# Performance work log

Hardware: AMD Instinct MI355X
Metric: run time of the kernel (lower is better)

## Reference

```python
import jax, jax.numpy as jnp
import numpy as np

N_QUBITS = 14
N_LAYERS = 4
N_CLASSES = 10
BATCH = 1024


def apply_1q(state, gate, wire):
    """Apply a 2x2 gate ([2,2] shared or [B,2,2] batched) to `wire` of state [B,2,...,2]."""
    s = jnp.moveaxis(state, wire + 1, -1)
    shp = s.shape
    s = s.reshape(shp[0], -1, 2)
    if gate.ndim == 3:
        s = jnp.einsum('bij,bkj->bki', gate, s)
    else:
        s = jnp.einsum('ij,bkj->bki', gate, s)
    return jnp.moveaxis(s.reshape(shp), -1, wire + 1)


def apply_cnot(state, c, t):
    s = jnp.moveaxis(state, (c + 1, t + 1), (-2, -1))
    s = jnp.stack([s[..., 0, :], s[..., 1, ::-1]], axis=-2)
    return jnp.moveaxis(s, (-2, -1), (c + 1, t + 1))


def simulate(x, q_params):
    """Batched statevector sim of: RY(x_i) embed -> BasicEntanglerLayers(RX + CNOT ring) -> <Z_i>."""
    B, n = x.shape
    state = jnp.zeros((B,) + (2,) * n, jnp.complex64)
    state = state.at[(slice(None),) + (0,) * n].set(1.0)

    # RY(x_i) on each wire (angles batched per sample)
    c, s = jnp.cos(0.5 * x), jnp.sin(0.5 * x)
    for w in range(n):
        g = jnp.stack([jnp.stack([c[:, w], -s[:, w]], -1),
                       jnp.stack([s[:, w], c[:, w]], -1)], -2).astype(jnp.complex64)  # [B,2,2]
        state = apply_1q(state, g, w)

    # BasicEntanglerLayers: per layer RX(weights[l,i]) on every wire, then CNOT ring
    cw, sw = jnp.cos(0.5 * q_params), jnp.sin(0.5 * q_params)
    n_layers = q_params.shape[0]
    for l in range(n_layers):
        for w in range(n):
            cc = cw[l, w].astype(jnp.complex64)
            isw = (-1j) * sw[l, w].astype(jnp.complex64)
            g = jnp.stack([jnp.stack([cc, isw]), jnp.stack([isw, cc])])  # [2,2] RX
            state = apply_1q(state, g, w)
        if n == 2:
            state = apply_cnot(state, 0, 1)
        else:
            for w in range(n):
                state = apply_cnot(state, w, (w + 1) % n)

    # <Z_i> = P(bit_i=0) - P(bit_i=1)
    p = jnp.abs(state) ** 2  # [B,2,...,2] real
    axes_all = tuple(range(1, n + 1))
    z = []
    for w in range(n):
        pw = jnp.sum(p, axis=tuple(a for a in axes_all if a != w + 1))  # [B,2]
        z.append(pw[:, 0] - pw[:, 1])
    return jnp.stack(z, -1).astype(jnp.float32)  # [B, n]


def setup_inputs() -> dict:
    key = jax.random.key(0)
    k1, k2, k3, k4 = jax.random.split(key, 4)
    x = jax.random.normal(k1, (BATCH, N_QUBITS), dtype=jnp.float32)
    q_params = 0.01 * jax.random.normal(k2, (N_LAYERS, N_QUBITS), dtype=jnp.float32)
    fc_w = jax.random.normal(k3, (N_CLASSES, N_QUBITS), dtype=jnp.float32) / np.sqrt(N_QUBITS)
    fc_b = jax.random.normal(k4, (N_CLASSES,), dtype=jnp.float32) * 0.01
    return {"x": x, "q_params": q_params, "fc_w": fc_w, "fc_b": fc_b}


def reference(x, q_params, fc_w, fc_b):
    q_out = simulate(x, q_params)            # [B, n_qubits]
    logits = q_out @ fc_w.T + fc_b           # [B, n_classes]
    return logits
```

## Files before the change

### kernel.cpp

```cpp
#include <hip/hip_runtime.h>
#include <hip/hip_fp16.h>
#include <math.h>


#define NQ 14
#define NLAYERS 4
#define NCLASSES 10
#define BLOCK 512

typedef _Float16 f16;
typedef _Float16 f16x2 __attribute__((ext_vector_type(2)));
typedef _Float16 f16x4 __attribute__((ext_vector_type(4)));
typedef _Float16 f16x8 __attribute__((ext_vector_type(8)));
typedef float f32x4 __attribute__((ext_vector_type(4)));
typedef unsigned int u32;
typedef u32 u32x2 __attribute__((ext_vector_type(2)));

__device__ __forceinline__ f32x4 mf(f16x8 a, f16x8 b, f32x4 c) {
  return __builtin_amdgcn_mfma_f32_16x16x32_f16(a, b, c, 0, 0, 0);
}
__device__ __forceinline__ f32x4 mf16(f16x4 a, f16x4 b, f32x4 c) {
  return __builtin_amdgcn_mfma_f32_16x16x16f16(a, b, c, 0, 0, 0);
}
__device__ __forceinline__ int swz(int t) { return ((t ^ (t >> 3)) & 7) << 3; }

__device__ __forceinline__ f16x4 cvt4(f32x4 v) {
  u32x2 r;
  r[0] = __builtin_bit_cast(u32, __builtin_amdgcn_cvt_pkrtz(v[0], v[1]));
  r[1] = __builtin_bit_cast(u32, __builtin_amdgcn_cvt_pkrtz(v[2], v[3]));
  return __builtin_bit_cast(f16x4, r);
}
__device__ __forceinline__ u32 dwof(f16x4 v, int k) {
  return __builtin_bit_cast(u32x2, v)[k];
}

__device__ __forceinline__ int finv5(int n) {
  n ^= ((n >> 3) & 1) << 4;
  n ^= ((n >> 2) & 1) << 3;
  n ^= ((n >> 1) & 1) << 2;
  n ^= (n & 1) << 1;
  return n;
}
__device__ __forceinline__ int finv3(int n) {
  n ^= ((n >> 2) & 1) << 3;
  n ^= ((n >> 1) & 1) << 2;
  n ^= (n & 1) << 1;
  return n;
}

__device__ __forceinline__ void build32(f16* Bc, const float* qc, const float* qs,
                                        int base, int tid) {
  const float c0 = qc[base], c1 = qc[base+1], c2 = qc[base+2], c3 = qc[base+3], c4 = qc[base+4];
  const float s0 = qs[base], s1 = qs[base+1], s2 = qs[base+2], s3 = qs[base+3], s4 = qs[base+4];
#pragma unroll
  for (int e = tid; e < 1024; e += BLOCK) {
    const int n = e >> 5, k = e & 31;
    const int d = finv5(n) ^ k;
    float mag = ((d & 1) ? s0 : c0) * ((d & 2) ? s1 : c1);
    mag *= ((d & 4) ? s2 : c2) * ((d & 8) ? s3 : c3);
    mag *= ((d & 16) ? s4 : c4);
    const int t = __popc(d) & 3;
    const f16 v = (f16)((t == 1 || t == 2) ? -mag : mag);
    const int p = 256 * (k >> 3) + 8 * n + (k & 7);
    const bool isreal = !(t & 1);
    Bc[p]        = isreal ? v : (f16)0.f;
    Bc[p + 1024] = isreal ? (f16)0.f : v;
  }
}

__device__ __forceinline__ void buildC2(f16* Cc, const float* qc, const float* qs,
                                        int base, int tid) {
  if (tid < 256) {
    const float c0 = qc[base], c1 = qc[base+1], c2 = qc[base+2], c3 = qc[base+3];
    const float s0 = qs[base], s1 = qs[base+1], s2 = qs[base+2], s3 = qs[base+3];
    const int rp = tid >> 4, k = tid & 15;
    const int d = finv3(rp) ^ k;
    float mag = ((d & 1) ? s0 : c0) * ((d & 2) ? s1 : c1);
    mag *= ((d & 4) ? s2 : c2) * ((d & 8) ? s3 : c3);
    const int t = __popc(d) & 3;
    const f16 v = (f16)((t == 1 || t == 2) ? -mag : mag);
    const bool isreal = !(t & 1);
    const int p = 16 * rp + k;
    Cc[p]       = isreal ? v : (f16)0.f;
    Cc[p + 256] = isreal ? (f16)0.f : v;
    Cc[p + 512] = isreal ? (f16)0.f : (f16)(-v);
  }
}

__device__ __forceinline__ void passA(f16* __restrict__ reP, f16* __restrict__ imP,
                                      const f16* __restrict__ BcR,
                                      f16* __restrict__ BcW, int baseB,
                                      f16* __restrict__ CcW, int baseC,
                                      const float* __restrict__ qc,
                                      const float* __restrict__ qs, int tid) {
  const int lane = tid & 63, wave = tid >> 6;
  const int q = lane >> 4, cc = lane & 15;
  const int n0 = cc, n1 = cc | 16;
  const f16x8 br0 = *(const f16x8*)(BcR + 256 * q + 8 * n0);
  const f16x8 bi0 = *(const f16x8*)(BcR + 1024 + 256 * q + 8 * n0);
  const f16x8 br1 = *(const f16x8*)(BcR + 256 * q + 8 * n1);
  const f16x8 bi1 = *(const f16x8*)(BcR + 1024 + 256 * q + 8 * n1);
  f16x8 Ar[4], Ai[4];
#pragma unroll
  for (int i = 0; i < 4; ++i) {
    const int mt = wave * 4 + i;
    const int pA = mt * 512 + ((128 * q + 8 * cc) ^ swz(mt));
    Ar[i] = *(const f16x8*)(reP + pA);
    Ai[i] = *(const f16x8*)(imP + pA);
  }
  __syncthreads();
  f16x4 outR[8], outI[8];
#pragma unroll
  for (int i = 0; i < 4; ++i) {
    const f16x8 nAi = -Ai[i];
    {
      f32x4 aR = {0.f,0.f,0.f,0.f}, aI = {0.f,0.f,0.f,0.f};
      aR = mf(Ar[i], br0, aR); aR = mf(nAi, bi0, aR);
      aI = mf(Ar[i], bi0, aI); aI = mf(Ai[i], br0, aI);
      outR[i * 2 + 0] = cvt4(aR);
      outI[i * 2 + 0] = cvt4(aI);
    }
    {
      f32x4 aR = {0.f,0.f,0.f,0.f}, aI = {0.f,0.f,0.f,0.f};
      aR = mf(Ar[i], br1, aR); aR = mf(nAi, bi1, aR);
      aI = mf(Ar[i], bi1, aI); aI = mf(Ai[i], br1, aI);
      outR[i * 2 + 1] = cvt4(aR);
      outI[i * 2 + 1] = cvt4(aI);
    }
  }
#pragma unroll
  for (int i = 0; i < 4; ++i) {
    const int mt = wave * 4 + i;
#pragma unroll
    for (int nt = 0; nt < 2; ++nt) {
      const int n5 = nt * 16 + cc;
      const int pS = n5 * 512 +
          ((128 * (2 * (mt & 1) + (q >> 1)) + 8 * (mt >> 1) + 4 * (q & 1)) ^ swz(n5));
      *(f16x4*)(reP + pS) = outR[i * 2 + nt];
      *(f16x4*)(imP + pS) = outI[i * 2 + nt];
    }
  }
  build32(BcW, qc, qs, baseB, tid);
  buildC2(CcW, qc, qs, baseC, tid);
}

template<bool FINAL>
__device__ __forceinline__ void superBC(f16* __restrict__ reP, f16* __restrict__ imP,
                                        const f16* __restrict__ BcR,
                                        const f16* __restrict__ Cc,
                                        f16* __restrict__ BcW, int baseB,
                                        const float* __restrict__ qc,
                                        const float* __restrict__ qs,
                                        int tid, float* __restrict__ zloc) {
  const int lane = tid & 63, wave = tid >> 6;
  const int q = lane >> 4, cc = lane & 15;
  int n0 = cc, n1 = cc | 16;
  if (wave >= 4) { n0 ^= 31; n1 ^= 31; }
  const f16x8 br0 = *(const f16x8*)(BcR + 256 * q + 8 * n0);
  const f16x8 bi0 = *(const f16x8*)(BcR + 1024 + 256 * q + 8 * n0);
  const f16x8 br1 = *(const f16x8*)(BcR + 256 * q + 8 * n1);
  const f16x8 bi1 = *(const f16x8*)(BcR + 1024 + 256 * q + 8 * n1);
  const int r0 = 16 * cc + 4 * q, r1 = 16 * (cc ^ 15) + 4 * q;
  const f16x4 ucr0 = *(const f16x4*)(Cc + r0);
  const f16x4 uci0 = *(const f16x4*)(Cc + 256 + r0);
  const f16x4 ucn0 = *(const f16x4*)(Cc + 512 + r0);
  const f16x4 ucr1 = *(const f16x4*)(Cc + r1);
  const f16x4 uci1 = *(const f16x4*)(Cc + 256 + r1);
  const f16x4 ucn1 = *(const f16x4*)(Cc + 512 + r1);
  f16x8 Ar[4], Ai[4];
#pragma unroll
  for (int i = 0; i < 4; ++i) {
    const int mt = wave * 4 + i;
    const int pA = mt * 512 + ((128 * q + 8 * cc) ^ swz(mt));
    Ar[i] = *(const f16x8*)(reP + pA);
    Ai[i] = *(const f16x8*)(imP + pA);
  }
  if constexpr (!FINAL) __syncthreads();

  f16x4 accR[4][2], accI[4][2];
  float z0b = 0.f, z1b = 0.f, z9b = 0.f, zA = 0.f, zB = 0.f, pt = 0.f;
#pragma unroll
  for (int i = 0; i < 4; ++i) {
    const f16x8 nAi = -Ai[i];
#pragma unroll
    for (int h = 0; h < 2; ++h) {
      const f16x8 br = h ? br1 : br0;
      const f16x8 bi = h ? bi1 : bi0;
      f32x4 aR = {0.f,0.f,0.f,0.f}, aI = {0.f,0.f,0.f,0.f};
      aR = mf(Ar[i], br, aR); aR = mf(nAi, bi, aR);
      aI = mf(Ar[i], bi, aI); aI = mf(Ai[i], br, aI);
      const f16x4 s1r = cvt4(aR), s1i = cvt4(aI);
      const f16x4 ur = h ? ucr1 : ucr0;
      const f16x4 ui = h ? uci1 : uci0;
      const f16x4 un = h ? ucn1 : ucn0;
      f32x4 cR = {0.f,0.f,0.f,0.f}, cI = {0.f,0.f,0.f,0.f};
      cR = mf16(ur, s1r, cR); cR = mf16(un, s1i, cR);
      cI = mf16(ui, s1r, cI); cI = mf16(ur, s1i, cI);
      if constexpr (FINAL) {
        const float p0 = cR[0]*cR[0] + cI[0]*cI[0];
        const float p1 = cR[1]*cR[1] + cI[1]*cI[1];
        const float p2 = cR[2]*cR[2] + cI[2]*cI[2];
        const float p3 = cR[3]*cR[3] + cI[3]*cI[3];
        const float ps = (p0 + p1) + (p2 + p3);
        zA += (p0 - p1) + (p2 - p3);
        zB += (p0 + p1) - (p2 + p3);
        z0b += (i & 1) ? -ps : ps;
        z1b += (i & 2) ? -ps : ps;
        z9b += h ? -ps : ps;
        pt  += ps;
      } else {
        accR[i][h] = cvt4(cR);
        accI[i][h] = cvt4(cI);
      }
    }
  }
  if constexpr (FINAL) {
    zloc[0]  += (q & 2) ? -z0b : z0b;
    zloc[1]  += z1b;
    zloc[2]  += (wave & 1) ? -pt : pt;
    zloc[3]  += (wave & 2) ? -pt : pt;
    zloc[4]  += (wave & 4) ? -pt : pt;
    zloc[5]  += (cc & 1) ? -pt : pt;
    zloc[6]  += (cc & 2) ? -pt : pt;
    zloc[7]  += (cc & 4) ? -pt : pt;
    zloc[8]  += (cc & 8) ? -pt : pt;
    zloc[9]  += z9b;
    zloc[10] += zA;
    zloc[11] += zB;
    zloc[12] += (q & 1) ? -pt : pt;
    zloc[13] += (q & 2) ? -pt : pt;
  } else {
    const u32 selLo = (q & 2) ? 0x01000504u : 0x05040100u;
    const u32 selHi = (q & 2) ? 0x03020706u : 0x07060302u;
    const int ibase = 128 * (wave >> 1) + 4 * (wave & 1);
#pragma unroll
    for (int h = 0; h < 2; ++h) {
#pragma unroll
      for (int j = 0; j < 4; ++j) {
        const int pS = (8 * q + 2 * j + h) * 512 + ibase +
                       8 * (cc ^ (2 * j + h) ^ q);
        const int dj = j >> 1;
        const u32 sel = (j & 1) ? selHi : selLo;
        u32x2 vr, vi;
        vr[0] = __builtin_amdgcn_perm(dwof(accR[1][h], dj), dwof(accR[0][h], dj), sel);
        vr[1] = __builtin_amdgcn_perm(dwof(accR[3][h], dj), dwof(accR[2][h], dj), sel);
        vi[0] = __builtin_amdgcn_perm(dwof(accI[1][h], dj), dwof(accI[0][h], dj), sel);
        vi[1] = __builtin_amdgcn_perm(dwof(accI[3][h], dj), dwof(accI[2][h], dj), sel);
        *(u32x2*)(reP + pS) = vr;
        *(u32x2*)(imP + pS) = vi;
      }
    }
    build32(BcW, qc, qs, baseB, tid);
  }
}

__global__ __launch_bounds__(BLOCK, 4) void qsim_kernel(
    const float* __restrict__ x, const float* __restrict__ qp,
    const float* __restrict__ fcw, const float* __restrict__ fcb,
    float* __restrict__ out) {
  extern __shared__ unsigned char smem[];
  f16* reP = (f16*)smem;
  f16* imP = reP + 16384;
  f16* Bc0 = imP + 16384;
  f16* Bc1 = Bc0 + 2048;
  f16* Cc  = Bc1 + 2048;
  float* qc = (float*)(Cc + 768);
  float* qs = qc + 56;
  float* xc = qs + 56;
  float* xs = xc + 14;

  const int b = blockIdx.x;
  const int tid = threadIdx.x;

  if (tid < NQ) {
    float sv, cv; sincosf(0.5f * x[b * NQ + tid], &sv, &cv);
    xc[tid] = cv; xs[tid] = sv;
  } else if (tid >= 64 && tid < 64 + NLAYERS * NQ) {
    const int k = tid - 64;
    float sv, cv; sincosf(0.5f * qp[k], &sv, &cv);
    qc[k] = cv; qs[k] = sv;
  }
  __syncthreads();

  float* Flo  = (float*)Bc0;
  float* psi  = Flo + 32;
  float* PsiR = psi + 32;
  float* PsiI = PsiR + 32;
  if (tid < 32) {
    float f = 1.f;
#pragma unroll
    for (int j = 0; j < 5; ++j) f *= ((tid >> j) & 1) ? xs[5 + j] : xc[5 + j];
    Flo[tid] = f;
  } else if (tid < 64) {
    const int k = tid - 32;
    float f = 1.f;
#pragma unroll
    for (int j = 0; j < 5; ++j) f *= ((k >> j) & 1) ? xs[j] : xc[j];
    psi[k] = f;
  }
  __syncthreads();
  if (tid < 32) {
    const float c0 = qc[0], c1 = qc[1], c2 = qc[2], c3 = qc[3], c4 = qc[4];
    const float s0 = qs[0], s1 = qs[1], s2 = qs[2], s3 = qs[3], s4 = qs[4];
    const int a = finv5(tid);
    float ar = 0.f, ai = 0.f;
    for (int k = 0; k < 32; ++k) {
      const int d = a ^ k;
      float mag = ((d & 1) ? s0 : c0) * ((d & 2) ? s1 : c1);
      mag *= ((d & 4) ? s2 : c2) * ((d & 8) ? s3 : c3);
      mag *= ((d & 16) ? s4 : c4);
      mag *= psi[k];
      const int t = __popc(d) & 3;
      if (t == 0) ar += mag; else if (t == 1) ai -= mag;
      else if (t == 2) ar -= mag; else ai += mag;
    }
    PsiR[tid] = ar; PsiI[tid] = ai;
  }
  __syncthreads();
  {
    float fhi = 1.f;
#pragma unroll
    for (int j = 0; j < 4; ++j) fhi *= ((tid >> j) & 1) ? xs[10 + j] : xc[10 + j];
    const float cr = fhi * PsiR[tid >> 4], ci = fhi * PsiI[tid >> 4];
    const int t = tid >> 4;
    const int sz = swz(t);
    float Fl[32];
#pragma unroll
    for (int j = 0; j < 32; ++j) Fl[j] = Flo[j];
    __syncthreads();
#pragma unroll
    for (int kb = 0; kb < 4; ++kb) {
      f16x8 hr, hi;
#pragma unroll
      for (int j = 0; j < 8; ++j) {
        const float F = Fl[8 * kb + j];
        hr[j] = (f16)(F * cr);
        hi[j] = (f16)(F * ci);
      }
      const int pb = t * 512 + ((128 * kb + 8 * (tid & 15)) ^ sz);
      *(f16x8*)(reP + pb) = hr;
      *(f16x8*)(imP + pb) = hi;
    }
  }
  build32(Bc0, qc, qs, 0 * NQ + 5, tid);
  buildC2(Cc, qc, qs, 0 * NQ + 10, tid);
  __syncthreads();

  superBC<false>(reP, imP, Bc0, Cc, Bc1, 1 * NQ + 0, qc, qs, tid, nullptr);
  __syncthreads();
#pragma unroll
  for (int l = 1; l < NLAYERS; ++l) {
    passA(reP, imP, Bc1, Bc0, l * NQ + 5, Cc, l * NQ + 10, qc, qs, tid);
    __syncthreads();
    if (l < NLAYERS - 1) {
      superBC<false>(reP, imP, Bc0, Cc, Bc1, (l + 1) * NQ + 0, qc, qs, tid, nullptr);
      __syncthreads();
    }
  }

  float zloc[NQ];
#pragma unroll
  for (int w = 0; w < NQ; ++w) zloc[w] = 0.f;
  superBC<true>(reP, imP, Bc0, Cc, nullptr, 0, qc, qs, tid, zloc);
  __syncthreads();

  float* zpart = (float*)Bc0;
  float* zbuf  = zpart + 112;
#pragma unroll
  for (int w = 0; w < NQ; ++w) {
#pragma unroll
    for (int off = 32; off > 0; off >>= 1)
      zloc[w] += __shfl_down(zloc[w], off, 64);
  }
  const int wave = tid >> 6, lane = tid & 63;
  if (lane == 0) {
#pragma unroll
    for (int w = 0; w < NQ; ++w) zpart[wave * NQ + w] = zloc[w];
  }
  __syncthreads();
  if (tid < NQ) {
    float a = 0.f;
#pragma unroll
    for (int v = 0; v < 8; ++v) a += zpart[v * NQ + tid];
    zbuf[tid] = a;
  }
  __syncthreads();
  if (tid < NCLASSES) {
    float acc = fcb[tid];
#pragma unroll
    for (int w = 0; w < NQ; ++w) acc = fmaf(zbuf[w], fcw[tid * NQ + w], acc);
    out[b * NCLASSES + tid] = acc;
  }
}

extern "C" void kernel_launch(void* const* d_in, const int* in_sizes, int n_in,
                              void* d_out, int out_size, void* d_ws, size_t ws_size,
                              hipStream_t stream) {
  const float* x   = (const float*)d_in[0];
  const float* qp  = (const float*)d_in[1];
  const float* fcw = (const float*)d_in[2];
  const float* fcb = (const float*)d_in[3];
  float* out = (float*)d_out;
  const int B = in_sizes[0] / NQ;

  const size_t shmem = (size_t)(2 * 16384 + 2 * 2048 + 768) * sizeof(f16)
                     + (size_t)(56 + 56 + 14 + 14) * sizeof(float);
  (void)hipFuncSetAttribute((const void*)qsim_kernel,
                            hipFuncAttributeMaxDynamicSharedMemorySize, (int)shmem);
  qsim_kernel<<<B, BLOCK, shmem, stream>>>(x, qp, fcw, fcb, out);
}
```

Measured before the change: 120.5 us.

## Precompute gate matrices in a prologue kernel and load them from global

Moves construction of the batch-independent RX gate matrices (B and C blocks) out of every block into a single-block prologue kernel that writes them to workspace. The main kernel then loads each layer's operands straight from global memory into registers, prefetching the next layer's operands during the current pass. This removes redundant per-block trig and matrix building plus the shared-memory staging, and cuts the LDS footprint, which may allow more blocks per CU. In exchange it adds a second kernel launch and global loads on the critical path.

```diff
diff --git a/kernel.cpp b/kernel.cpp
--- a/kernel.cpp
+++ b/kernel.cpp
@@ -48,58 +48,89 @@
   return n;
 }
 
-__device__ __forceinline__ void build32(f16* Bc, const float* qc, const float* qs,
-                                        int base, int tid) {
-  const float c0 = qc[base], c1 = qc[base+1], c2 = qc[base+2], c3 = qc[base+3], c4 = qc[base+4];
-  const float s0 = qs[base], s1 = qs[base+1], s2 = qs[base+2], s3 = qs[base+3], s4 = qs[base+4];
+__global__ void qsim_build(const float* __restrict__ qp,
+                           f16* __restrict__ gB, f16* __restrict__ gC) {
+  __shared__ float qc[NLAYERS * NQ], qs[NLAYERS * NQ];
+  const int tid = threadIdx.x;
+  if (tid < NLAYERS * NQ) {
+    float sv, cv; sincosf(0.5f * qp[tid], &sv, &cv);
+    qc[tid] = cv; qs[tid] = sv;
+  }
+  __syncthreads();
+#pragma unroll
+  for (int p = 0; p < 7; ++p) {
+    const int l = (p + 1) >> 1;
+    const int base = 14 * l + ((p & 1) ? 0 : 5);
+    const float c0 = qc[base], c1 = qc[base+1], c2 = qc[base+2], c3 = qc[base+3], c4 = qc[base+4];
+    const float s0 = qs[base], s1 = qs[base+1], s2 = qs[base+2], s3 = qs[base+3], s4 = qs[base+4];
+#pragma unroll
+    for (int e = tid; e < 1024; e += BLOCK) {
+      const int n = e >> 5, k = e & 31;
+      const int d = finv5(n) ^ k;
+      float mag = ((d & 1) ? s0 : c0) * ((d & 2) ? s1 : c1);
+      mag *= ((d & 4) ? s2 : c2) * ((d & 8) ? s3 : c3);
+      mag *= ((d & 16) ? s4 : c4);
+      const int t = __popc(d) & 3;
+      const f16 v = (f16)((t == 1 || t == 2) ? -mag : mag);
+      const int pp = 256 * (k >> 3) + 8 * n + (k & 7);
+      const bool isreal = !(t & 1);
+      gB[p * 2048 + pp]        = isreal ? v : (f16)0.f;
+      gB[p * 2048 + pp + 1024] = isreal ? (f16)0.f : v;
+    }
+  }
 #pragma unroll
   for (int e = tid; e < 1024; e += BLOCK) {
-    const int n = e >> 5, k = e & 31;
-    const int d = finv5(n) ^ k;
-    float mag = ((d & 1) ? s0 : c0) * ((d & 2) ? s1 : c1);
-    mag *= ((d & 4) ? s2 : c2) * ((d & 8) ? s3 : c3);
-    mag *= ((d & 16) ? s4 : c4);
-    const int t = __popc(d) & 3;
-    const f16 v = (f16)((t == 1 || t == 2) ? -mag : mag);
-    const int p = 256 * (k >> 3) + 8 * n + (k & 7);
-    const bool isreal = !(t & 1);
-    Bc[p]        = isreal ? v : (f16)0.f;
-    Bc[p + 1024] = isreal ? (f16)0.f : v;
-  }
-}
-
-__device__ __forceinline__ void buildC2(f16* Cc, const float* qc, const float* qs,
-                                        int base, int tid) {
-  if (tid < 256) {
+    const int li = e >> 8, rp = (e >> 4) & 15, k = e & 15;
+    const int base = 14 * li + 10;
     const float c0 = qc[base], c1 = qc[base+1], c2 = qc[base+2], c3 = qc[base+3];
     const float s0 = qs[base], s1 = qs[base+1], s2 = qs[base+2], s3 = qs[base+3];
-    const int rp = tid >> 4, k = tid & 15;
     const int d = finv3(rp) ^ k;
     float mag = ((d & 1) ? s0 : c0) * ((d & 2) ? s1 : c1);
     mag *= ((d & 4) ? s2 : c2) * ((d & 8) ? s3 : c3);
     const int t = __popc(d) & 3;
     const f16 v = (f16)((t == 1 || t == 2) ? -mag : mag);
     const bool isreal = !(t & 1);
-    const int p = 16 * rp + k;
-    Cc[p]       = isreal ? v : (f16)0.f;
-    Cc[p + 256] = isreal ? (f16)0.f : v;
-    Cc[p + 512] = isreal ? (f16)0.f : (f16)(-v);
-  }
-}
-
-__device__ __forceinline__ void passA(f16* __restrict__ reP, f16* __restrict__ imP,
-                                      const f16* __restrict__ BcR,
-                                      f16* __restrict__ BcW, int baseB,
-                                      f16* __restrict__ CcW, int baseC,
-                                      const float* __restrict__ qc,
-                                      const float* __restrict__ qs, int tid) {
+    const int pp = li * 512 + 16 * rp + k;
+    gC[pp]       = isreal ? v : (f16)0.f;
+    gC[pp + 256] = isreal ? (f16)0.f : v;
+  }
+}
+
+struct FB { f16x8 br0, bi0, br1, bi1; };
+struct FC { f16x4 ur0, ui0, ur1, ui1; };
+
+__device__ __forceinline__ FB loadB(const f16* __restrict__ g, bool ctrl, int tid) {
   const int lane = tid & 63, wave = tid >> 6;
   const int q = lane >> 4, cc = lane & 15;
-  const int n0 = cc, n1 = cc | 16;
-  const f16x8 br0 = *(const f16x8*)(BcR + 256 * q + 8 * n0);
-  const f16x8 bi0 = *(const f16x8*)(BcR + 1024 + 256 * q + 8 * n0);
-  const f16x8 br1 = *(const f16x8*)(BcR + 256 * q + 8 * n1);
-  const f16x8 bi1 = *(const f16x8*)(BcR + 1024 + 256 * q + 8 * n1);
+  int n0 = cc, n1 = cc | 16;
+  if (ctrl && wave >= 4) { n0 ^= 31; n1 ^= 31; }
+  FB f;
+  f.br0 = *(const f16x8*)(g + 256 * q + 8 * n0);
+  f.bi0 = *(const f16x8*)(g + 1024 + 256 * q + 8 * n0);
+  f.br1 = *(const f16x8*)(g + 256 * q + 8 * n1);
+  f.bi1 = *(const f16x8*)(g + 1024 + 256 * q + 8 * n1);
+  return f;
+}
+__device__ __forceinline__ FC loadC(const f16* __restrict__ g, int tid) {
+  const int lane = tid & 63;
+  const int q = lane >> 4, cc = lane & 15;
+  const int r0 = 16 * cc + 4 * q, r1 = 16 * (cc ^ 15) + 4 * q;
+  FC f;
+  f.ur0 = *(const f16x4*)(g + r0);
+  f.ui0 = *(const f16x4*)(g + 256 + r0);
+  f.ur1 = *(const f16x4*)(g + r1);
+  f.ui1 = *(const f16x4*)(g + 256 + r1);
+  return f;
+}
+
+__device__ __forceinline__ void passA(f16* __restrict__ reP, f16* __restrict__ imP,
+                                      const FB fb,
+                                      const f16* __restrict__ gNB,
+                                      const f16* __restrict__ gNC,
+                                      FB* __restrict__ nextB,
+                                      FC* __restrict__ nextC, int tid) {
+  const int lane = tid & 63, wave = tid >> 6;
+  const int q = lane >> 4, cc = lane & 15;
   f16x8 Ar[4], Ai[4];
 #pragma unroll
   for (int i = 0; i < 4; ++i) {
@@ -109,21 +140,23 @@
     Ai[i] = *(const f16x8*)(imP + pA);
   }
   __syncthreads();
+  *nextB = loadB(gNB, true, tid);
+  *nextC = loadC(gNC, tid);
   f16x4 outR[8], outI[8];
 #pragma unroll
   for (int i = 0; i < 4; ++i) {
     const f16x8 nAi = -Ai[i];
     {
       f32x4 aR = {0.f,0.f,0.f,0.f}, aI = {0.f,0.f,0.f,0.f};
-      aR = mf(Ar[i], br0, aR); aR = mf(nAi, bi0, aR);
-      aI = mf(Ar[i], bi0, aI); aI = mf(Ai[i], br0, aI);
+      aR = mf(Ar[i], fb.br0, aR); aR = mf(nAi, fb.bi0, aR);
+      aI = mf(Ar[i], fb.bi0, aI); aI = mf(Ai[i], fb.br0, aI);
       outR[i * 2 + 0] = cvt4(aR);
       outI[i * 2 + 0] = cvt4(aI);
     }
     {
       f32x4 aR = {0.f,0.f,0.f,0.f}, aI = {0.f,0.f,0.f,0.f};
-      aR = mf(Ar[i], br1, aR); aR = mf(nAi, bi1, aR);
-      aI = mf(Ar[i], bi1, aI); aI = mf(Ai[i], br1, aI);
+      aR = mf(Ar[i], fb.br1, aR); aR = mf(nAi, fb.bi1, aR);
+      aI = mf(Ar[i], fb.bi1, aI); aI = mf(Ai[i], fb.br1, aI);
       outR[i * 2 + 1] = cvt4(aR);
       outI[i * 2 + 1] = cvt4(aI);
     }
@@ -140,33 +173,16 @@
       *(f16x4*)(imP + pS) = outI[i * 2 + nt];
     }
   }
-  build32(BcW, qc, qs, baseB, tid);
-  buildC2(CcW, qc, qs, baseC, tid);
 }
 
 template<bool FINAL>
 __device__ __forceinline__ void superBC(f16* __restrict__ reP, f16* __restrict__ imP,
-                                        const f16* __restrict__ BcR,
-                                        const f16* __restrict__ Cc,
-                                        f16* __restrict__ BcW, int baseB,
-                                        const float* __restrict__ qc,
-                                        const float* __restrict__ qs,
+                                        const FB fb, const FC fc,
+                                        const f16* __restrict__ gNB,
+                                        FB* __restrict__ nextB,
                                         int tid, float* __restrict__ zloc) {
   const int lane = tid & 63, wave = tid >> 6;
   const int q = lane >> 4, cc = lane & 15;
-  int n0 = cc, n1 = cc | 16;
-  if (wave >= 4) { n0 ^= 31; n1 ^= 31; }
-  const f16x8 br0 = *(const f16x8*)(BcR + 256 * q + 8 * n0);
-  const f16x8 bi0 = *(const f16x8*)(BcR + 1024 + 256 * q + 8 * n0);
-  const f16x8 br1 = *(const f16x8*)(BcR + 256 * q + 8 * n1);
-  const f16x8 bi1 = *(const f16x8*)(BcR + 1024 + 256 * q + 8 * n1);
-  const int r0 = 16 * cc + 4 * q, r1 = 16 * (cc ^ 15) + 4 * q;
-  const f16x4 ucr0 = *(const f16x4*)(Cc + r0);
-  const f16x4 uci0 = *(const f16x4*)(Cc + 256 + r0);
-  const f16x4 ucn0 = *(const f16x4*)(Cc + 512 + r0);
-  const f16x4 ucr1 = *(const f16x4*)(Cc + r1);
-  const f16x4 uci1 = *(const f16x4*)(Cc + 256 + r1);
-  const f16x4 ucn1 = *(const f16x4*)(Cc + 512 + r1);
   f16x8 Ar[4], Ai[4];
 #pragma unroll
   for (int i = 0; i < 4; ++i) {
@@ -175,7 +191,11 @@
     Ar[i] = *(const f16x8*)(reP + pA);
     Ai[i] = *(const f16x8*)(imP + pA);
   }
-  if constexpr (!FINAL) __syncthreads();
+  if constexpr (!FINAL) {
+    __syncthreads();
+    *nextB = loadB(gNB, false, tid);
+  }
+  const f16x4 ucn0 = -fc.ui0, ucn1 = -fc.ui1;
 
   f16x4 accR[4][2], accI[4][2];
   float z0b = 0.f, z1b = 0.f, z9b = 0.f, zA = 0.f, zB = 0.f, pt = 0.f;
@@ -184,14 +204,14 @@
     const f16x8 nAi = -Ai[i];
 #pragma unroll
     for (int h = 0; h < 2; ++h) {
-      const f16x8 br = h ? br1 : br0;
-      const f16x8 bi = h ? bi1 : bi0;
+      const f16x8 br = h ? fb.br1 : fb.br0;
+      const f16x8 bi = h ? fb.bi1 : fb.bi0;
       f32x4 aR = {0.f,0.f,0.f,0.f}, aI = {0.f,0.f,0.f,0.f};
       aR = mf(Ar[i], br, aR); aR = mf(nAi, bi, aR);
       aI = mf(Ar[i], bi, aI); aI = mf(Ai[i], br, aI);
       const f16x4 s1r = cvt4(aR), s1i = cvt4(aI);
-      const f16x4 ur = h ? ucr1 : ucr0;
-      const f16x4 ui = h ? uci1 : uci0;
+      const f16x4 ur = h ? fc.ur1 : fc.ur0;
+      const f16x4 ui = h ? fc.ui1 : fc.ui0;
       const f16x4 un = h ? ucn1 : ucn0;
       f32x4 cR = {0.f,0.f,0.f,0.f}, cI = {0.f,0.f,0.f,0.f};
       cR = mf16(ur, s1r, cR); cR = mf16(un, s1i, cR);
@@ -250,39 +270,40 @@
         *(u32x2*)(imP + pS) = vi;
       }
     }
-    build32(BcW, qc, qs, baseB, tid);
   }
 }
 
 __global__ __launch_bounds__(BLOCK, 4) void qsim_kernel(
     const float* __restrict__ x, const float* __restrict__ qp,
     const float* __restrict__ fcw, const float* __restrict__ fcb,
+    const f16* __restrict__ gB, const f16* __restrict__ gC,
     float* __restrict__ out) {
   extern __shared__ unsigned char smem[];
   f16* reP = (f16*)smem;
   f16* imP = reP + 16384;
-  f16* Bc0 = imP + 16384;
-  f16* Bc1 = Bc0 + 2048;
-  f16* Cc  = Bc1 + 2048;
-  float* qc = (float*)(Cc + 768);
-  float* qs = qc + 56;
-  float* xc = qs + 56;
-  float* xs = xc + 14;
+  float* scratch = (float*)(imP + 16384);
+  float* qc = scratch + 128;
+  float* qs = qc + 8;
+  float* xc = qs + 8;
+  float* xs = xc + 16;
 
   const int b = blockIdx.x;
   const int tid = threadIdx.x;
+
+  FB fb = loadB(gB, true, tid);
+  FC fc = loadC(gC, tid);
 
   if (tid < NQ) {
     float sv, cv; sincosf(0.5f * x[b * NQ + tid], &sv, &cv);
     xc[tid] = cv; xs[tid] = sv;
-  } else if (tid >= 64 && tid < 64 + NLAYERS * NQ) {
+  } else if (tid >= 64 && tid < 64 + 5) {
     const int k = tid - 64;
     float sv, cv; sincosf(0.5f * qp[k], &sv, &cv);
     qc[k] = cv; qs[k] = sv;
   }
   __syncthreads();
 
-  float* Flo  = (float*)Bc0;
+  float* Flo  = scratch;
   float* psi  = Flo + 32;
   float* PsiR = psi + 32;
   float* PsiI = PsiR + 32;
@@ -324,16 +345,12 @@
     const float cr = fhi * PsiR[tid >> 4], ci = fhi * PsiI[tid >> 4];
     const int t = tid >> 4;
     const int sz = swz(t);
-    float Fl[32];
-#pragma unroll
-    for (int j = 0; j < 32; ++j) Fl[j] = Flo[j];
-    __syncthreads();
 #pragma unroll
     for (int kb = 0; kb < 4; ++kb) {
       f16x8 hr, hi;
 #pragma unroll
       for (int j = 0; j < 8; ++j) {
-        const float F = Fl[8 * kb + j];
+        const float F = Flo[8 * kb + j];
         hr[j] = (f16)(F * cr);
         hi[j] = (f16)(F * ci);
       }
@@ -342,18 +359,17 @@
       *(f16x8*)(imP + pb) = hi;
     }
   }
-  build32(Bc0, qc, qs, 0 * NQ + 5, tid);
-  buildC2(Cc, qc, qs, 0 * NQ + 10, tid);
-  __syncthreads();
-
-  superBC<false>(reP, imP, Bc0, Cc, Bc1, 1 * NQ + 0, qc, qs, tid, nullptr);
+  __syncthreads();
+
+  FB fbN; FC fcN;
+  superBC<false>(reP, imP, fb, fc, gB + 1 * 2048, &fbN, tid, nullptr);
   __syncthreads();
 #pragma unroll
   for (int l = 1; l < NLAYERS; ++l) {
-    passA(reP, imP, Bc1, Bc0, l * NQ + 5, Cc, l * NQ + 10, qc, qs, tid);
+    passA(reP, imP, fbN, gB + (2 * l) * 2048, gC + l * 512, &fb, &fc, tid);
     __syncthreads();
     if (l < NLAYERS - 1) {
-      superBC<false>(reP, imP, Bc0, Cc, Bc1, (l + 1) * NQ + 0, qc, qs, tid, nullptr);
+      superBC<false>(reP, imP, fb, fc, gB + (2 * l + 1) * 2048, &fbN, tid, nullptr);
       __syncthreads();
     }
   }
@@ -361,10 +377,10 @@
   float zloc[NQ];
 #pragma unroll
   for (int w = 0; w < NQ; ++w) zloc[w] = 0.f;
-  superBC<true>(reP, imP, Bc0, Cc, nullptr, 0, qc, qs, tid, zloc);
-  __syncthreads();
-
-  float* zpart = (float*)Bc0;
+  superBC<true>(reP, imP, fb, fc, nullptr, nullptr, tid, zloc);
+  __syncthreads();
+
+  float* zpart = scratch;
   float* zbuf  = zpart + 112;
 #pragma unroll
   for (int w = 0; w < NQ; ++w) {
@@ -403,9 +419,14 @@
   float* out = (float*)d_out;
   const int B = in_sizes[0] / NQ;
 
-  const size_t shmem = (size_t)(2 * 16384 + 2 * 2048 + 768) * sizeof(f16)
-                     + (size_t)(56 + 56 + 14 + 14) * sizeof(float);
+  f16* gB = (f16*)d_ws;
+  f16* gC = gB + 7 * 2048;
+
+  qsim_build<<<1, BLOCK, 0, stream>>>(qp, gB, gC);
+
+  const size_t shmem = (size_t)(2 * 16384) * sizeof(f16)
+                     + (size_t)(128 + 8 + 8 + 16 + 16) * sizeof(float);
   (void)hipFuncSetAttribute((const void*)qsim_kernel,
                             hipFuncAttributeMaxDynamicSharedMemorySize, (int)shmem);
-  qsim_kernel<<<B, BLOCK, shmem, stream>>>(x, qp, fcw, fcb, out);
-}
+  qsim_kernel<<<B, BLOCK, shmem, stream>>>(x, qp, fcw, fcb, gB, gC, out);
+}
```

After: 119.5 us (median of 2 runs). No clear change (-0.8%).
